# Performance work log

Hardware: AMD Instinct MI355X
Metric: run time of the kernel (lower is better)

Reference implementation:

```python
import jax, jax.numpy as jnp
import numpy as np

B, S, D = 4, 2048, 1024
H, HD = 16, 64
ROT_DIM = 64
ROT_BASE = 10000.0


def setup_inputs() -> dict:
    key = jax.random.key(0)
    ks = jax.random.split(key, 5)
    return {
        "hidden_states": jax.random.normal(ks[0], (B, S, D), dtype=jnp.float32),
        "Wqkv_w": jax.random.normal(ks[1], (3 * D, D), dtype=jnp.float32) * 0.02,
        "Wqkv_b": jax.random.normal(ks[2], (3 * D,), dtype=jnp.float32) * 0.02,
        "Wo_w": jax.random.normal(ks[3], (D, D), dtype=jnp.float32) * 0.02,
        "Wo_b": jax.random.normal(ks[4], (D,), dtype=jnp.float32) * 0.02,
    }


def _rope_cos_sin(seqlen, dtype):
    inv_freq = 1.0 / (ROT_BASE ** (jnp.arange(0, ROT_DIM, 2, dtype=jnp.float32) / ROT_DIM))
    t = jnp.arange(seqlen, dtype=jnp.float32)
    freqs = jnp.einsum("s,f->sf", t, inv_freq)  # (S, ROT_DIM//2)
    return jnp.cos(freqs).astype(dtype), jnp.sin(freqs).astype(dtype)


def _apply_rope(x, cos, sin):
    # x: (B, S, H, HD), non-interleaved rotary on first ROT_DIM dims
    ro, pas = x[..., :ROT_DIM], x[..., ROT_DIM:]
    x1, x2 = ro[..., : ROT_DIM // 2], ro[..., ROT_DIM // 2 :]
    c = cos[None, :, None, :]  # (1, S, 1, ROT_DIM//2)
    s = sin[None, :, None, :]
    rot = jnp.concatenate([x1 * c - x2 * s, x1 * s + x2 * c], axis=-1)
    return jnp.concatenate([rot, pas], axis=-1) if pas.shape[-1] else rot


def reference(hidden_states, Wqkv_w, Wqkv_b, Wo_w, Wo_b):
    b, s, d = hidden_states.shape
    qkv = hidden_states @ Wqkv_w.T + Wqkv_b  # (B, S, 3D)
    qkv = qkv.reshape(b, s, 3, H, HD)
    q, k, v = qkv[:, :, 0], qkv[:, :, 1], qkv[:, :, 2]  # each (B, S, H, HD)
    cos, sin = _rope_cos_sin(s, hidden_states.dtype)
    q = _apply_rope(q, cos, sin)
    k = _apply_rope(k, cos, sin)
    scale = 1.0 / jnp.sqrt(jnp.asarray(HD, hidden_states.dtype))
    scores = jnp.einsum("bqhd,bkhd->bhqk", q, k) * scale
    probs = jax.nn.softmax(scores, axis=-1)
    attn = jnp.einsum("bhqk,bkhd->bqhd", probs, v)  # (B, S, H, HD)
    attn = attn.reshape(b, s, d)
    return attn @ Wo_w.T + Wo_b
```

## Files before the change

### kernel.cpp

```cpp
#include <hip/hip_runtime.h>
#include <hip/hip_bf16.h>
#include <cstdint>
#include <cstddef>

typedef __bf16 bf16;
typedef __bf16 bf16x4 __attribute__((ext_vector_type(4)));
typedef __bf16 bf16x8 __attribute__((ext_vector_type(8)));
typedef float f32x4 __attribute__((ext_vector_type(4)));

#define NB 4
#define NS 2048
#define ND 1024
#define NH 16
#define NHD 64
#define NM (NB * NS)

__device__ inline void lds_dma16(const bf16* g, bf16* l) {
    __builtin_amdgcn_global_load_lds(
        (const __attribute__((address_space(1))) void*)g,
        (__attribute__((address_space(3))) void*)l, 16, 0, 0);
}

__global__ void rope_table_kernel(float* __restrict__ cost, float* __restrict__ sint) {
    int i = blockIdx.x * 256 + threadIdx.x;
    int s = i >> 5, f = i & 31;
    float inv = exp2f(-(float)f * (13.287712379549449f / 32.0f));
    float ang = (float)s * inv;
    cost[i] = cosf(ang);
    sint[i] = sinf(ang);
}

__global__ void cvt_bf16_kernel(const float4* __restrict__ in, bf16x4* __restrict__ out) {
    int i = blockIdx.x * 256 + threadIdx.x;
    float4 v = in[i];
    bf16x4 r = {(bf16)v.x, (bf16)v.y, (bf16)v.z, (bf16)v.w};
    out[i] = r;
}

__global__ void __launch_bounds__(256) qkv_rope_gemm(
    const bf16* __restrict__ A, const bf16* __restrict__ W,
    const float* __restrict__ bias,
    const float* __restrict__ cost, const float* __restrict__ sint,
    bf16* __restrict__ Qw, bf16* __restrict__ Kw, bf16* __restrict__ Vt) {
    __shared__ __attribute__((aligned(16))) bf16 lA[128 * 32];
    __shared__ __attribute__((aligned(16))) bf16 lB[128 * 32];

    int t = threadIdx.x, lane = t & 63, w = t >> 6;
    int col = lane & 15, quad = lane >> 4;
    int m0 = blockIdx.y * 128, n0 = blockIdx.x * 128;
    int wm = (w >> 1) * 64, wn = (w & 1) * 64;

    f32x4 acc[4][4];
#pragma unroll
    for (int i = 0; i < 4; ++i)
#pragma unroll
        for (int j = 0; j < 4; ++j) acc[i][j] = (f32x4){0.f, 0.f, 0.f, 0.f};

    const bf16* gA0 = A + (size_t)(m0 + w * 32 + (lane >> 2)) * ND + (lane & 3) * 8;
    const bf16* gA1 = gA0 + (size_t)16 * ND;
    const bf16* gB0 = W + (size_t)(n0 + w * 32 + (lane >> 2)) * ND + (lane & 3) * 8;
    const bf16* gB1 = gB0 + (size_t)16 * ND;
    bf16* ldsA0 = &lA[(w * 32) * 32];
    bf16* ldsA1 = &lA[(w * 32 + 16) * 32];
    bf16* ldsB0 = &lB[(w * 32) * 32];
    bf16* ldsB1 = &lB[(w * 32 + 16) * 32];

    for (int kt = 0; kt < ND; kt += 32) {
        lds_dma16(gA0 + kt, ldsA0);
        lds_dma16(gA1 + kt, ldsA1);
        lds_dma16(gB0 + kt, ldsB0);
        lds_dma16(gB1 + kt, ldsB1);
        __syncthreads();
        bf16x8 af[4], bg[4];
#pragma unroll
        for (int i = 0; i < 4; ++i)
            af[i] = *(const bf16x8*)&lA[(wm + i * 16 + col) * 32 + quad * 8];
#pragma unroll
        for (int j = 0; j < 4; ++j)
            bg[j] = *(const bf16x8*)&lB[(wn + j * 16 + col) * 32 + quad * 8];
#pragma unroll
        for (int i = 0; i < 4; ++i)
#pragma unroll
            for (int j = 0; j < 4; ++j)
                acc[i][j] = __builtin_amdgcn_mfma_f32_16x16x32_bf16(af[i], bg[j], acc[i][j], 0, 0, 0);
        __syncthreads();
    }

    int nseg = n0 + wn;
    int which = nseg >> 10;
    int h = (nseg >> 6) & (NH - 1);
    float bj[4];
#pragma unroll
    for (int j = 0; j < 4; ++j) bj[j] = bias[nseg + j * 16 + col];

#pragma unroll
    for (int i = 0; i < 4; ++i) {
#pragma unroll
        for (int r = 0; r < 4; ++r) {
            int m = m0 + wm + i * 16 + quad * 4 + r;
            int b = m >> 11, s = m & (NS - 1);
            float v0 = acc[i][0][r] + bj[0];
            float v1 = acc[i][1][r] + bj[1];
            float v2 = acc[i][2][r] + bj[2];
            float v3 = acc[i][3][r] + bj[3];
            if (which == 2) {
                bf16* dst = Vt + (size_t)(b * NH + h) * NHD * NS;
                dst[(size_t)(col) * NS + s] = (bf16)v0;
                dst[(size_t)(16 + col) * NS + s] = (bf16)v1;
                dst[(size_t)(32 + col) * NS + s] = (bf16)v2;
                dst[(size_t)(48 + col) * NS + s] = (bf16)v3;
            } else {
                bf16* dst = (which ? Kw : Qw) + ((size_t)(b * NH + h) * NS + s) * NHD;
                float c0 = cost[s * 32 + col], s0 = sint[s * 32 + col];
                float c1 = cost[s * 32 + 16 + col], s1 = sint[s * 32 + 16 + col];
                dst[col] = (bf16)(v0 * c0 - v2 * s0);
                dst[16 + col] = (bf16)(v1 * c1 - v3 * s1);
                dst[32 + col] = (bf16)(v0 * s0 + v2 * c0);
                dst[48 + col] = (bf16)(v1 * s1 + v3 * c1);
            }
        }
    }
}

__global__ void __launch_bounds__(256, 4) attn_kernel(
    const bf16* __restrict__ Qw, const bf16* __restrict__ Kw,
    const bf16* __restrict__ Vt, bf16* __restrict__ X) {
    const int LDK = 72;
    const int LV = 40;
    __shared__ __attribute__((aligned(16))) bf16 lK[32 * LDK];
    __shared__ __attribute__((aligned(16))) bf16 lV[64 * LV];

    int t = threadIdx.x, lane = t & 63, w = t >> 6;
    int col = lane & 15, q = lane >> 4;
    int bh = blockIdx.y, b = bh >> 4, h = bh & 15;
    int q0 = blockIdx.x * 128 + w * 32;
    const bf16* Qh = Qw + (size_t)bh * NS * NHD;
    const bf16* Kh = Kw + (size_t)bh * NS * NHD;
    const bf16* Vh = Vt + (size_t)bh * NHD * NS;

    int krow = t >> 3, kc = t & 7;
    int vrow = t >> 2, vc = t & 3;
    const bf16* gK = Kh + (size_t)krow * NHD + kc * 8;
    const bf16* gV = Vh + (size_t)vrow * NS + vc * 8;
    bf16* wK = &lK[krow * LDK + kc * 8];
    bf16* wV = &lV[vrow * LV + vc * 8];

    bf16x8 bQ[2][2];
#pragma unroll
    for (int mb = 0; mb < 2; ++mb)
#pragma unroll
        for (int h2 = 0; h2 < 2; ++h2)
            bQ[mb][h2] = *(const bf16x8*)(Qh + (size_t)(q0 + mb * 16 + col) * NHD + h2 * 32 + q * 8);

    f32x4 o[2][4];
#pragma unroll
    for (int mb = 0; mb < 2; ++mb)
#pragma unroll
        for (int hb = 0; hb < 4; ++hb) o[mb][hb] = (f32x4){0.f, 0.f, 0.f, 0.f};
    float dsum[2] = {0.f, 0.f};

    bf16x8 kreg = *(const bf16x8*)gK;
    bf16x8 vreg = *(const bf16x8*)gV;

    for (int kt = 0; kt < NS; kt += 32) {
        *(bf16x8*)wK = kreg;
        *(bf16x8*)wV = vreg;
        __syncthreads();
        if (kt + 32 < NS) {
            kreg = *(const bf16x8*)(gK + (size_t)(kt + 32) * NHD);
            vreg = *(const bf16x8*)(gV + kt + 32);
        }

        bf16x8 aK[2][2];
#pragma unroll
        for (int tb = 0; tb < 2; ++tb)
#pragma unroll
            for (int h2 = 0; h2 < 2; ++h2)
                aK[tb][h2] = *(const bf16x8*)&lK[(tb * 16 + col) * LDK + h2 * 32 + q * 8];
        bf16x8 vf[4];
#pragma unroll
        for (int hb = 0; hb < 4; ++hb) {
            const bf16* vr = &lV[(hb * 16 + col) * LV + q * 4];
            bf16x4 lo = *(const bf16x4*)vr;
            bf16x4 hi = *(const bf16x4*)(vr + 16);
            vf[hb] = __builtin_shufflevector(lo, hi, 0, 1, 2, 3, 4, 5, 6, 7);
        }
#pragma unroll
        for (int mb = 0; mb < 2; ++mb) {
            f32x4 s0 = (f32x4){0.f, 0.f, 0.f, 0.f};
            f32x4 s1 = (f32x4){0.f, 0.f, 0.f, 0.f};
            s0 = __builtin_amdgcn_mfma_f32_16x16x32_bf16(aK[0][0], bQ[mb][0], s0, 0, 0, 0);
            s0 = __builtin_amdgcn_mfma_f32_16x16x32_bf16(aK[0][1], bQ[mb][1], s0, 0, 0, 0);
            s1 = __builtin_amdgcn_mfma_f32_16x16x32_bf16(aK[1][0], bQ[mb][0], s1, 0, 0, 0);
            s1 = __builtin_amdgcn_mfma_f32_16x16x32_bf16(aK[1][1], bQ[mb][1], s1, 0, 0, 0);
            bf16x8 pf;
            float ds = 0.f;
#pragma unroll
            for (int r = 0; r < 4; ++r) {
                float p0 = __expf(s0[r] * 0.125f);
                float p1 = __expf(s1[r] * 0.125f);
                pf[r] = (bf16)p0;
                pf[4 + r] = (bf16)p1;
                ds += p0 + p1;
            }
            dsum[mb] += ds;
#pragma unroll
            for (int hb = 0; hb < 4; ++hb)
                o[mb][hb] = __builtin_amdgcn_mfma_f32_16x16x32_bf16(vf[hb], pf, o[mb][hb], 0, 0, 0);
        }
        __syncthreads();
    }

#pragma unroll
    for (int mb = 0; mb < 2; ++mb) {
        dsum[mb] += __shfl_xor(dsum[mb], 16);
        dsum[mb] += __shfl_xor(dsum[mb], 32);
        float linv = 1.0f / dsum[mb];
        int s = q0 + mb * 16 + col;
        bf16* dst = X + (size_t)(b * NS + s) * ND + h * NHD;
#pragma unroll
        for (int hb = 0; hb < 4; ++hb) {
            bf16x4 ov = {(bf16)(o[mb][hb][0] * linv), (bf16)(o[mb][hb][1] * linv),
                         (bf16)(o[mb][hb][2] * linv), (bf16)(o[mb][hb][3] * linv)};
            *(bf16x4*)(dst + hb * 16 + q * 4) = ov;
        }
    }
}

__global__ void __launch_bounds__(256) out_gemm(
    const bf16* __restrict__ A, const bf16* __restrict__ W,
    const float* __restrict__ bias, float* __restrict__ out) {
    __shared__ __attribute__((aligned(16))) bf16 lA[128 * 32];
    __shared__ __attribute__((aligned(16))) bf16 lB[128 * 32];

    int t = threadIdx.x, lane = t & 63, w = t >> 6;
    int col = lane & 15, quad = lane >> 4;
    int m0 = blockIdx.y * 128, n0 = blockIdx.x * 128;
    int wm = (w >> 1) * 64, wn = (w & 1) * 64;

    f32x4 acc[4][4];
#pragma unroll
    for (int i = 0; i < 4; ++i)
#pragma unroll
        for (int j = 0; j < 4; ++j) acc[i][j] = (f32x4){0.f, 0.f, 0.f, 0.f};

    const bf16* gA0 = A + (size_t)(m0 + w * 32 + (lane >> 2)) * ND + (lane & 3) * 8;
    const bf16* gA1 = gA0 + (size_t)16 * ND;
    const bf16* gB0 = W + (size_t)(n0 + w * 32 + (lane >> 2)) * ND + (lane & 3) * 8;
    const bf16* gB1 = gB0 + (size_t)16 * ND;
    bf16* ldsA0 = &lA[(w * 32) * 32];
    bf16* ldsA1 = &lA[(w * 32 + 16) * 32];
    bf16* ldsB0 = &lB[(w * 32) * 32];
    bf16* ldsB1 = &lB[(w * 32 + 16) * 32];

    for (int kt = 0; kt < ND; kt += 32) {
        lds_dma16(gA0 + kt, ldsA0);
        lds_dma16(gA1 + kt, ldsA1);
        lds_dma16(gB0 + kt, ldsB0);
        lds_dma16(gB1 + kt, ldsB1);
        __syncthreads();
        bf16x8 af[4], bg[4];
#pragma unroll
        for (int i = 0; i < 4; ++i)
            af[i] = *(const bf16x8*)&lA[(wm + i * 16 + col) * 32 + quad * 8];
#pragma unroll
        for (int j = 0; j < 4; ++j)
            bg[j] = *(const bf16x8*)&lB[(wn + j * 16 + col) * 32 + quad * 8];
#pragma unroll
        for (int i = 0; i < 4; ++i)
#pragma unroll
            for (int j = 0; j < 4; ++j)
                acc[i][j] = __builtin_amdgcn_mfma_f32_16x16x32_bf16(af[i], bg[j], acc[i][j], 0, 0, 0);
        __syncthreads();
    }

    float bj[4];
#pragma unroll
    for (int j = 0; j < 4; ++j) bj[j] = bias[n0 + wn + j * 16 + col];
#pragma unroll
    for (int i = 0; i < 4; ++i)
#pragma unroll
        for (int r = 0; r < 4; ++r) {
            int m = m0 + wm + i * 16 + quad * 4 + r;
#pragma unroll
            for (int j = 0; j < 4; ++j)
                out[(size_t)m * ND + n0 + wn + j * 16 + col] = acc[i][j][r] + bj[j];
        }
}

extern "C" void kernel_launch(void* const* d_in, const int* in_sizes, int n_in,
                              void* d_out, int out_size, void* d_ws, size_t ws_size,
                              hipStream_t stream) {
    const float* hs = (const float*)d_in[0];
    const float* Wqkv = (const float*)d_in[1];
    const float* bqkv = (const float*)d_in[2];
    const float* Wo = (const float*)d_in[3];
    const float* bo = (const float*)d_in[4];
    float* out = (float*)d_out;

    char* ws = (char*)d_ws;
    float* cost = (float*)ws;
    float* sint = cost + NS * 32;
    bf16* Qw = (bf16*)(ws + 524288);
    bf16* Kw = Qw + (size_t)NB * NH * NS * NHD;
    bf16* Vt = Kw + (size_t)NB * NH * NS * NHD;
    bf16* X = Vt + (size_t)NB * NH * NS * NHD;
    bf16* Wqkv_b = (bf16*)d_out;
    bf16* Wo_b = Qw;

    rope_table_kernel<<<dim3(NS * 32 / 256), dim3(256), 0, stream>>>(cost, sint);
    cvt_bf16_kernel<<<dim3(NM * ND / 4 / 256), dim3(256), 0, stream>>>(
        (const float4*)hs, (bf16x4*)X);
    cvt_bf16_kernel<<<dim3(3 * ND * ND / 4 / 256), dim3(256), 0, stream>>>(
        (const float4*)Wqkv, (bf16x4*)Wqkv_b);
    qkv_rope_gemm<<<dim3(3 * ND / 128, NM / 128), dim3(256), 0, stream>>>(
        X, Wqkv_b, bqkv, cost, sint, Qw, Kw, Vt);
    attn_kernel<<<dim3(NS / 128, NB * NH), dim3(256), 0, stream>>>(Qw, Kw, Vt, X);
    cvt_bf16_kernel<<<dim3(ND * ND / 4 / 256), dim3(256), 0, stream>>>(
        (const float4*)Wo, (bf16x4*)Wo_b);
    out_gemm<<<dim3(ND / 128, NM / 128), dim3(256), 0, stream>>>(X, Wo_b, bo, out);
}
```

Baseline: 304.1 us.

## Double-buffer LDS in GEMMs and attention, widen attention query tile per wave

Both GEMMs get two LDS stages, so the DMA for the next k-tile is issued before the MFMAs on the current tile, and one barrier per iteration is dropped. The attention kernel double-buffers K/V in LDS with register prefetch two tiles ahead, keeping a single barrier per iteration. Each wave now handles 64 queries instead of 32, so each loaded K/V tile is reused across more queries. This costs more registers, launch bounds drop to 2 blocks per CU, and the grid is half as large, which may reduce occupancy and latency hiding.

```diff
diff --git a/kernel.cpp b/kernel.cpp
--- a/kernel.cpp
+++ b/kernel.cpp
@@ -42,8 +42,8 @@
     const float* __restrict__ bias,
     const float* __restrict__ cost, const float* __restrict__ sint,
     bf16* __restrict__ Qw, bf16* __restrict__ Kw, bf16* __restrict__ Vt) {
-    __shared__ __attribute__((aligned(16))) bf16 lA[128 * 32];
-    __shared__ __attribute__((aligned(16))) bf16 lB[128 * 32];
+    __shared__ __attribute__((aligned(16))) bf16 lA[2][128 * 32];
+    __shared__ __attribute__((aligned(16))) bf16 lB[2][128 * 32];
 
     int t = threadIdx.x, lane = t & 63, w = t >> 6;
     int col = lane & 15, quad = lane >> 4;
@@ -60,29 +60,36 @@
     const bf16* gA1 = gA0 + (size_t)16 * ND;
     const bf16* gB0 = W + (size_t)(n0 + w * 32 + (lane >> 2)) * ND + (lane & 3) * 8;
     const bf16* gB1 = gB0 + (size_t)16 * ND;
-    bf16* ldsA0 = &lA[(w * 32) * 32];
-    bf16* ldsA1 = &lA[(w * 32 + 16) * 32];
-    bf16* ldsB0 = &lB[(w * 32) * 32];
-    bf16* ldsB1 = &lB[(w * 32 + 16) * 32];
-
-    for (int kt = 0; kt < ND; kt += 32) {
-        lds_dma16(gA0 + kt, ldsA0);
-        lds_dma16(gA1 + kt, ldsA1);
-        lds_dma16(gB0 + kt, ldsB0);
-        lds_dma16(gB1 + kt, ldsB1);
-        __syncthreads();
+    int ldsOff0 = (w * 32) * 32;
+    int ldsOff1 = (w * 32 + 16) * 32;
+
+    lds_dma16(gA0, &lA[0][ldsOff0]);
+    lds_dma16(gA1, &lA[0][ldsOff1]);
+    lds_dma16(gB0, &lB[0][ldsOff0]);
+    lds_dma16(gB1, &lB[0][ldsOff1]);
+    __syncthreads();
+
+    for (int i = 0; i < 32; ++i) {
+        int cur = i & 1, nxt = cur ^ 1;
+        if (i + 1 < 32) {
+            int kt = (i + 1) * 32;
+            lds_dma16(gA0 + kt, &lA[nxt][ldsOff0]);
+            lds_dma16(gA1 + kt, &lA[nxt][ldsOff1]);
+            lds_dma16(gB0 + kt, &lB[nxt][ldsOff0]);
+            lds_dma16(gB1 + kt, &lB[nxt][ldsOff1]);
+        }
         bf16x8 af[4], bg[4];
 #pragma unroll
-        for (int i = 0; i < 4; ++i)
-            af[i] = *(const bf16x8*)&lA[(wm + i * 16 + col) * 32 + quad * 8];
+        for (int ii = 0; ii < 4; ++ii)
+            af[ii] = *(const bf16x8*)&lA[cur][(wm + ii * 16 + col) * 32 + quad * 8];
 #pragma unroll
         for (int j = 0; j < 4; ++j)
-            bg[j] = *(const bf16x8*)&lB[(wn + j * 16 + col) * 32 + quad * 8];
-#pragma unroll
-        for (int i = 0; i < 4; ++i)
+            bg[j] = *(const bf16x8*)&lB[cur][(wn + j * 16 + col) * 32 + quad * 8];
+#pragma unroll
+        for (int ii = 0; ii < 4; ++ii)
 #pragma unroll
             for (int j = 0; j < 4; ++j)
-                acc[i][j] = __builtin_amdgcn_mfma_f32_16x16x32_bf16(af[i], bg[j], acc[i][j], 0, 0, 0);
+                acc[ii][j] = __builtin_amdgcn_mfma_f32_16x16x32_bf16(af[ii], bg[j], acc[ii][j], 0, 0, 0);
         __syncthreads();
     }
 
@@ -122,18 +129,18 @@
     }
 }
 
-__global__ void __launch_bounds__(256, 4) attn_kernel(
+__global__ void __launch_bounds__(256, 2) attn_kernel(
     const bf16* __restrict__ Qw, const bf16* __restrict__ Kw,
     const bf16* __restrict__ Vt, bf16* __restrict__ X) {
     const int LDK = 72;
     const int LV = 40;
-    __shared__ __attribute__((aligned(16))) bf16 lK[32 * LDK];
-    __shared__ __attribute__((aligned(16))) bf16 lV[64 * LV];
+    __shared__ __attribute__((aligned(16))) bf16 lK[2][32 * LDK];
+    __shared__ __attribute__((aligned(16))) bf16 lV[2][64 * LV];
 
     int t = threadIdx.x, lane = t & 63, w = t >> 6;
     int col = lane & 15, q = lane >> 4;
     int bh = blockIdx.y, b = bh >> 4, h = bh & 15;
-    int q0 = blockIdx.x * 128 + w * 32;
+    int q0 = blockIdx.x * 256 + w * 64;
     const bf16* Qh = Qw + (size_t)bh * NS * NHD;
     const bf16* Kh = Kw + (size_t)bh * NS * NHD;
     const bf16* Vh = Vt + (size_t)bh * NHD * NS;
@@ -142,33 +149,38 @@
     int vrow = t >> 2, vc = t & 3;
     const bf16* gK = Kh + (size_t)krow * NHD + kc * 8;
     const bf16* gV = Vh + (size_t)vrow * NS + vc * 8;
-    bf16* wK = &lK[krow * LDK + kc * 8];
-    bf16* wV = &lV[vrow * LV + vc * 8];
-
-    bf16x8 bQ[2][2];
-#pragma unroll
-    for (int mb = 0; mb < 2; ++mb)
+    int wKoff = krow * LDK + kc * 8;
+    int wVoff = vrow * LV + vc * 8;
+
+    bf16x8 bQ[4][2];
+#pragma unroll
+    for (int mb = 0; mb < 4; ++mb)
 #pragma unroll
         for (int h2 = 0; h2 < 2; ++h2)
             bQ[mb][h2] = *(const bf16x8*)(Qh + (size_t)(q0 + mb * 16 + col) * NHD + h2 * 32 + q * 8);
 
-    f32x4 o[2][4];
-#pragma unroll
-    for (int mb = 0; mb < 2; ++mb)
+    f32x4 o[4][4];
+#pragma unroll
+    for (int mb = 0; mb < 4; ++mb)
 #pragma unroll
         for (int hb = 0; hb < 4; ++hb) o[mb][hb] = (f32x4){0.f, 0.f, 0.f, 0.f};
-    float dsum[2] = {0.f, 0.f};
-
-    bf16x8 kreg = *(const bf16x8*)gK;
-    bf16x8 vreg = *(const bf16x8*)gV;
-
-    for (int kt = 0; kt < NS; kt += 32) {
-        *(bf16x8*)wK = kreg;
-        *(bf16x8*)wV = vreg;
+    float dsum[4] = {0.f, 0.f, 0.f, 0.f};
+
+    bf16x8 kr[2], vr[2];
+    kr[0] = *(const bf16x8*)gK;
+    vr[0] = *(const bf16x8*)gV;
+    kr[1] = *(const bf16x8*)(gK + (size_t)32 * NHD);
+    vr[1] = *(const bf16x8*)(gV + 32);
+    *(bf16x8*)&lK[0][wKoff] = kr[0];
+    *(bf16x8*)&lV[0][wVoff] = vr[0];
+
+#pragma unroll 2
+    for (int it = 0; it < 64; ++it) {
         __syncthreads();
-        if (kt + 32 < NS) {
-            kreg = *(const bf16x8*)(gK + (size_t)(kt + 32) * NHD);
-            vreg = *(const bf16x8*)(gV + kt + 32);
+        int cur = it & 1, nxt = cur ^ 1;
+        if (it + 2 < 64) {
+            kr[cur] = *(const bf16x8*)(gK + (size_t)(it + 2) * 32 * NHD);
+            vr[cur] = *(const bf16x8*)(gV + (it + 2) * 32);
         }
 
         bf16x8 aK[2][2];
@@ -176,17 +188,17 @@
         for (int tb = 0; tb < 2; ++tb)
 #pragma unroll
             for (int h2 = 0; h2 < 2; ++h2)
-                aK[tb][h2] = *(const bf16x8*)&lK[(tb * 16 + col) * LDK + h2 * 32 + q * 8];
+                aK[tb][h2] = *(const bf16x8*)&lK[cur][(tb * 16 + col) * LDK + h2 * 32 + q * 8];
         bf16x8 vf[4];
 #pragma unroll
         for (int hb = 0; hb < 4; ++hb) {
-            const bf16* vr = &lV[(hb * 16 + col) * LV + q * 4];
-            bf16x4 lo = *(const bf16x4*)vr;
-            bf16x4 hi = *(const bf16x4*)(vr + 16);
+            const bf16* vp = &lV[cur][(hb * 16 + col) * LV + q * 4];
+            bf16x4 lo = *(const bf16x4*)vp;
+            bf16x4 hi = *(const bf16x4*)(vp + 16);
             vf[hb] = __builtin_shufflevector(lo, hi, 0, 1, 2, 3, 4, 5, 6, 7);
         }
 #pragma unroll
-        for (int mb = 0; mb < 2; ++mb) {
+        for (int mb = 0; mb < 4; ++mb) {
             f32x4 s0 = (f32x4){0.f, 0.f, 0.f, 0.f};
             f32x4 s1 = (f32x4){0.f, 0.f, 0.f, 0.f};
             s0 = __builtin_amdgcn_mfma_f32_16x16x32_bf16(aK[0][0], bQ[mb][0], s0, 0, 0, 0);
@@ -208,11 +220,15 @@
             for (int hb = 0; hb < 4; ++hb)
                 o[mb][hb] = __builtin_amdgcn_mfma_f32_16x16x32_bf16(vf[hb], pf, o[mb][hb], 0, 0, 0);
         }
-        __syncthreads();
-    }
-
-#pragma unroll
-    for (int mb = 0; mb < 2; ++mb) {
+
+        if (it + 1 < 64) {
+            *(bf16x8*)&lK[nxt][wKoff] = kr[nxt];
+            *(bf16x8*)&lV[nxt][wVoff] = vr[nxt];
+        }
+    }
+
+#pragma unroll
+    for (int mb = 0; mb < 4; ++mb) {
         dsum[mb] += __shfl_xor(dsum[mb], 16);
         dsum[mb] += __shfl_xor(dsum[mb], 32);
         float linv = 1.0f / dsum[mb];
@@ -230,8 +246,8 @@
 __global__ void __launch_bounds__(256) out_gemm(
     const bf16* __restrict__ A, const bf16* __restrict__ W,
     const float* __restrict__ bias, float* __restrict__ out) {
-    __shared__ __attribute__((aligned(16))) bf16 lA[128 * 32];
-    __shared__ __attribute__((aligned(16))) bf16 lB[128 * 32];
+    __shared__ __attribute__((aligned(16))) bf16 lA[2][128 * 32];
+    __shared__ __attribute__((aligned(16))) bf16 lB[2][128 * 32];
 
     int t = threadIdx.x, lane = t & 63, w = t >> 6;
     int col = lane & 15, quad = lane >> 4;
@@ -248,29 +264,36 @@
     const bf16* gA1 = gA0 + (size_t)16 * ND;
     const bf16* gB0 = W + (size_t)(n0 + w * 32 + (lane >> 2)) * ND + (lane & 3) * 8;
     const bf16* gB1 = gB0 + (size_t)16 * ND;
-    bf16* ldsA0 = &lA[(w * 32) * 32];
-    bf16* ldsA1 = &lA[(w * 32 + 16) * 32];
-    bf16* ldsB0 = &lB[(w * 32) * 32];
-    bf16* ldsB1 = &lB[(w * 32 + 16) * 32];
-
-    for (int kt = 0; kt < ND; kt += 32) {
-        lds_dma16(gA0 + kt, ldsA0);
-        lds_dma16(gA1 + kt, ldsA1);
-        lds_dma16(gB0 + kt, ldsB0);
-        lds_dma16(gB1 + kt, ldsB1);
-        __syncthreads();
+    int ldsOff0 = (w * 32) * 32;
+    int ldsOff1 = (w * 32 + 16) * 32;
+
+    lds_dma16(gA0, &lA[0][ldsOff0]);
+    lds_dma16(gA1, &lA[0][ldsOff1]);
+    lds_dma16(gB0, &lB[0][ldsOff0]);
+    lds_dma16(gB1, &lB[0][ldsOff1]);
+    __syncthreads();
+
+    for (int i = 0; i < 32; ++i) {
+        int cur = i & 1, nxt = cur ^ 1;
+        if (i + 1 < 32) {
+            int kt = (i + 1) * 32;
+            lds_dma16(gA0 + kt, &lA[nxt][ldsOff0]);
+            lds_dma16(gA1 + kt, &lA[nxt][ldsOff1]);
+            lds_dma16(gB0 + kt, &lB[nxt][ldsOff0]);
+            lds_dma16(gB1 + kt, &lB[nxt][ldsOff1]);
+        }
         bf16x8 af[4], bg[4];
 #pragma unroll
-        for (int i = 0; i < 4; ++i)
-            af[i] = *(const bf16x8*)&lA[(wm + i * 16 + col) * 32 + quad * 8];
+        for (int ii = 0; ii < 4; ++ii)
+            af[ii] = *(const bf16x8*)&lA[cur][(wm + ii * 16 + col) * 32 + quad * 8];
 #pragma unroll
         for (int j = 0; j < 4; ++j)
-            bg[j] = *(const bf16x8*)&lB[(wn + j * 16 + col) * 32 + quad * 8];
-#pragma unroll
-        for (int i = 0; i < 4; ++i)
+            bg[j] = *(const bf16x8*)&lB[cur][(wn + j * 16 + col) * 32 + quad * 8];
+#pragma unroll
+        for (int ii = 0; ii < 4; ++ii)
 #pragma unroll
             for (int j = 0; j < 4; ++j)
-                acc[i][j] = __builtin_amdgcn_mfma_f32_16x16x32_bf16(af[i], bg[j], acc[i][j], 0, 0, 0);
+                acc[ii][j] = __builtin_amdgcn_mfma_f32_16x16x32_bf16(af[ii], bg[j], acc[ii][j], 0, 0, 0);
         __syncthreads();
     }
 
@@ -315,7 +338,7 @@
         (const float4*)Wqkv, (bf16x4*)Wqkv_b);
     qkv_rope_gemm<<<dim3(3 * ND / 128, NM / 128), dim3(256), 0, stream>>>(
         X, Wqkv_b, bqkv, cost, sint, Qw, Kw, Vt);
-    attn_kernel<<<dim3(NS / 128, NB * NH), dim3(256), 0, stream>>>(Qw, Kw, Vt, X);
+    attn_kernel<<<dim3(NS / 256, NB * NH), dim3(256), 0, stream>>>(Qw, Kw, Vt, X);
     cvt_bf16_kernel<<<dim3(ND * ND / 4 / 256), dim3(256), 0, stream>>>(
         (const float4*)Wo, (bf16x4*)Wo_b);
     out_gemm<<<dim3(ND / 128, NM / 128), dim3(256), 0, stream>>>(X, Wo_b, bo, out);
```

Result: slower. 312.3 us (+2.7%).

## Double-buffer attention K/V tiles, widen query tile per wave, vectorize V stores

Applied to the files above, without the earlier changes.

The attention kernel now gives each wave 64 queries instead of 32, so every K/V tile staged in LDS feeds twice as many MFMAs. It double-buffers LDS with a two-deep register prefetch, which leaves one barrier per iteration instead of two. The grid is halved and launch bounds drop to 2 blocks per CU because of the higher register pressure. Separately, the QKV GEMM epilogue writes the transposed V as packed 4-element bf16 vectors instead of scalar stores. The risks are lower occupancy and fewer blocks (512) in flight to hide latency.

```diff
diff --git a/kernel.cpp b/kernel.cpp
--- a/kernel.cpp
+++ b/kernel.cpp
@@ -93,23 +93,31 @@
 #pragma unroll
     for (int j = 0; j < 4; ++j) bj[j] = bias[nseg + j * 16 + col];
 
-#pragma unroll
-    for (int i = 0; i < 4; ++i) {
-#pragma unroll
-        for (int r = 0; r < 4; ++r) {
-            int m = m0 + wm + i * 16 + quad * 4 + r;
-            int b = m >> 11, s = m & (NS - 1);
-            float v0 = acc[i][0][r] + bj[0];
-            float v1 = acc[i][1][r] + bj[1];
-            float v2 = acc[i][2][r] + bj[2];
-            float v3 = acc[i][3][r] + bj[3];
-            if (which == 2) {
-                bf16* dst = Vt + (size_t)(b * NH + h) * NHD * NS;
-                dst[(size_t)(col) * NS + s] = (bf16)v0;
-                dst[(size_t)(16 + col) * NS + s] = (bf16)v1;
-                dst[(size_t)(32 + col) * NS + s] = (bf16)v2;
-                dst[(size_t)(48 + col) * NS + s] = (bf16)v3;
-            } else {
+    if (which == 2) {
+        int mbase = m0 + wm;
+        int b = mbase >> 11;
+        bf16* dsth = Vt + (size_t)(b * NH + h) * NHD * NS;
+#pragma unroll
+        for (int i = 0; i < 4; ++i) {
+            int s = ((mbase + i * 16) & (NS - 1)) + quad * 4;
+#pragma unroll
+            for (int j = 0; j < 4; ++j) {
+                bf16x4 pv = {(bf16)(acc[i][j][0] + bj[j]), (bf16)(acc[i][j][1] + bj[j]),
+                             (bf16)(acc[i][j][2] + bj[j]), (bf16)(acc[i][j][3] + bj[j])};
+                *(bf16x4*)(dsth + (size_t)(j * 16 + col) * NS + s) = pv;
+            }
+        }
+    } else {
+#pragma unroll
+        for (int i = 0; i < 4; ++i) {
+#pragma unroll
+            for (int r = 0; r < 4; ++r) {
+                int m = m0 + wm + i * 16 + quad * 4 + r;
+                int b = m >> 11, s = m & (NS - 1);
+                float v0 = acc[i][0][r] + bj[0];
+                float v1 = acc[i][1][r] + bj[1];
+                float v2 = acc[i][2][r] + bj[2];
+                float v3 = acc[i][3][r] + bj[3];
                 bf16* dst = (which ? Kw : Qw) + ((size_t)(b * NH + h) * NS + s) * NHD;
                 float c0 = cost[s * 32 + col], s0 = sint[s * 32 + col];
                 float c1 = cost[s * 32 + 16 + col], s1 = sint[s * 32 + 16 + col];
@@ -122,18 +130,18 @@
     }
 }
 
-__global__ void __launch_bounds__(256, 4) attn_kernel(
+__global__ void __launch_bounds__(256, 2) attn_kernel(
     const bf16* __restrict__ Qw, const bf16* __restrict__ Kw,
     const bf16* __restrict__ Vt, bf16* __restrict__ X) {
     const int LDK = 72;
     const int LV = 40;
-    __shared__ __attribute__((aligned(16))) bf16 lK[32 * LDK];
-    __shared__ __attribute__((aligned(16))) bf16 lV[64 * LV];
+    __shared__ __attribute__((aligned(16))) bf16 lK[2][32 * LDK];
+    __shared__ __attribute__((aligned(16))) bf16 lV[2][64 * LV];
 
     int t = threadIdx.x, lane = t & 63, w = t >> 6;
     int col = lane & 15, q = lane >> 4;
     int bh = blockIdx.y, b = bh >> 4, h = bh & 15;
-    int q0 = blockIdx.x * 128 + w * 32;
+    int q0 = blockIdx.x * 256 + w * 64;
     const bf16* Qh = Qw + (size_t)bh * NS * NHD;
     const bf16* Kh = Kw + (size_t)bh * NS * NHD;
     const bf16* Vh = Vt + (size_t)bh * NHD * NS;
@@ -142,33 +150,38 @@
     int vrow = t >> 2, vc = t & 3;
     const bf16* gK = Kh + (size_t)krow * NHD + kc * 8;
     const bf16* gV = Vh + (size_t)vrow * NS + vc * 8;
-    bf16* wK = &lK[krow * LDK + kc * 8];
-    bf16* wV = &lV[vrow * LV + vc * 8];
-
-    bf16x8 bQ[2][2];
-#pragma unroll
-    for (int mb = 0; mb < 2; ++mb)
+    int wKoff = krow * LDK + kc * 8;
+    int wVoff = vrow * LV + vc * 8;
+
+    bf16x8 bQ[4][2];
+#pragma unroll
+    for (int mb = 0; mb < 4; ++mb)
 #pragma unroll
         for (int h2 = 0; h2 < 2; ++h2)
             bQ[mb][h2] = *(const bf16x8*)(Qh + (size_t)(q0 + mb * 16 + col) * NHD + h2 * 32 + q * 8);
 
-    f32x4 o[2][4];
-#pragma unroll
-    for (int mb = 0; mb < 2; ++mb)
+    f32x4 o[4][4];
+#pragma unroll
+    for (int mb = 0; mb < 4; ++mb)
 #pragma unroll
         for (int hb = 0; hb < 4; ++hb) o[mb][hb] = (f32x4){0.f, 0.f, 0.f, 0.f};
-    float dsum[2] = {0.f, 0.f};
-
-    bf16x8 kreg = *(const bf16x8*)gK;
-    bf16x8 vreg = *(const bf16x8*)gV;
-
-    for (int kt = 0; kt < NS; kt += 32) {
-        *(bf16x8*)wK = kreg;
-        *(bf16x8*)wV = vreg;
-        __syncthreads();
-        if (kt + 32 < NS) {
-            kreg = *(const bf16x8*)(gK + (size_t)(kt + 32) * NHD);
-            vreg = *(const bf16x8*)(gV + kt + 32);
+    float dsum[4] = {0.f, 0.f, 0.f, 0.f};
+
+    bf16x8 kr[2], vr[2];
+    kr[0] = *(const bf16x8*)gK;
+    vr[0] = *(const bf16x8*)gV;
+    kr[1] = *(const bf16x8*)(gK + (size_t)32 * NHD);
+    vr[1] = *(const bf16x8*)(gV + 32);
+    *(bf16x8*)&lK[0][wKoff] = kr[0];
+    *(bf16x8*)&lV[0][wVoff] = vr[0];
+
+#pragma unroll 2
+    for (int it = 0; it < 64; ++it) {
+        __syncthreads();
+        int cur = it & 1, nxt = cur ^ 1;
+        if (it + 2 < 64) {
+            kr[cur] = *(const bf16x8*)(gK + (size_t)(it + 2) * 32 * NHD);
+            vr[cur] = *(const bf16x8*)(gV + (it + 2) * 32);
         }
 
         bf16x8 aK[2][2];
@@ -176,17 +189,17 @@
         for (int tb = 0; tb < 2; ++tb)
 #pragma unroll
             for (int h2 = 0; h2 < 2; ++h2)
-                aK[tb][h2] = *(const bf16x8*)&lK[(tb * 16 + col) * LDK + h2 * 32 + q * 8];
+                aK[tb][h2] = *(const bf16x8*)&lK[cur][(tb * 16 + col) * LDK + h2 * 32 + q * 8];
         bf16x8 vf[4];
 #pragma unroll
         for (int hb = 0; hb < 4; ++hb) {
-            const bf16* vr = &lV[(hb * 16 + col) * LV + q * 4];
-            bf16x4 lo = *(const bf16x4*)vr;
-            bf16x4 hi = *(const bf16x4*)(vr + 16);
+            const bf16* vp = &lV[cur][(hb * 16 + col) * LV + q * 4];
+            bf16x4 lo = *(const bf16x4*)vp;
+            bf16x4 hi = *(const bf16x4*)(vp + 16);
             vf[hb] = __builtin_shufflevector(lo, hi, 0, 1, 2, 3, 4, 5, 6, 7);
         }
 #pragma unroll
-        for (int mb = 0; mb < 2; ++mb) {
+        for (int mb = 0; mb < 4; ++mb) {
             f32x4 s0 = (f32x4){0.f, 0.f, 0.f, 0.f};
             f32x4 s1 = (f32x4){0.f, 0.f, 0.f, 0.f};
             s0 = __builtin_amdgcn_mfma_f32_16x16x32_bf16(aK[0][0], bQ[mb][0], s0, 0, 0, 0);
@@ -208,11 +221,15 @@
             for (int hb = 0; hb < 4; ++hb)
                 o[mb][hb] = __builtin_amdgcn_mfma_f32_16x16x32_bf16(vf[hb], pf, o[mb][hb], 0, 0, 0);
         }
-        __syncthreads();
-    }
-
-#pragma unroll
-    for (int mb = 0; mb < 2; ++mb) {
+
+        if (it + 1 < 64) {
+            *(bf16x8*)&lK[nxt][wKoff] = kr[nxt];
+            *(bf16x8*)&lV[nxt][wVoff] = vr[nxt];
+        }
+    }
+
+#pragma unroll
+    for (int mb = 0; mb < 4; ++mb) {
         dsum[mb] += __shfl_xor(dsum[mb], 16);
         dsum[mb] += __shfl_xor(dsum[mb], 32);
         float linv = 1.0f / dsum[mb];
@@ -315,7 +332,7 @@
         (const float4*)Wqkv, (bf16x4*)Wqkv_b);
     qkv_rope_gemm<<<dim3(3 * ND / 128, NM / 128), dim3(256), 0, stream>>>(
         X, Wqkv_b, bqkv, cost, sint, Qw, Kw, Vt);
-    attn_kernel<<<dim3(NS / 128, NB * NH), dim3(256), 0, stream>>>(Qw, Kw, Vt, X);
+    attn_kernel<<<dim3(NS / 256, NB * NH), dim3(256), 0, stream>>>(Qw, Kw, Vt, X);
     cvt_bf16_kernel<<<dim3(ND * ND / 4 / 256), dim3(256), 0, stream>>>(
         (const float4*)Wo, (bf16x4*)Wo_b);
     out_gemm<<<dim3(ND / 128, NM / 128), dim3(256), 0, stream>>>(X, Wo_b, bo, out);
```

New measurement: 291.3 us. 1.04x faster.
